# Kernel tuning notes

Hardware: AMD Instinct MI355X
Metric: run time of the kernel (lower is better)

The kernel has to match this reference:

```python
import jax, jax.numpy as jnp
import numpy as np

CUBE_SIZE = 24
N_NEURONS = CUBE_SIZE ** 3  # 13824
INPUT_DIM = 512
OUTPUT_DIM = 1000
MAX_STEPS = 30
BATCH = 256


def _build_neighbor_indices(size: int) -> np.ndarray:
    """[N, 27] int32; invalid (out-of-cube) neighbors map to pad slot N."""
    n = size ** 3
    c = np.arange(size)
    z, y, x = np.meshgrid(c, c, c, indexing='ij')  # each [size,size,size]
    cols = []
    for dz in (-1, 0, 1):
        for dy in (-1, 0, 1):
            for dx in (-1, 0, 1):
                nz, ny, nx = z + dz, y + dy, x + dx
                valid = ((nz >= 0) & (nz < size) & (ny >= 0) & (ny < size)
                         & (nx >= 0) & (nx < size))
                idx = nz * size * size + ny * size + nx
                cols.append(np.where(valid, idx, n))
    return np.stack(cols, axis=-1).reshape(n, 27).astype(np.int32)


def setup_inputs() -> dict:
    key = jax.random.key(0)
    ks = jax.random.split(key, 4)
    # xavier-ish small init scales (gain 0.5 style)
    w_in = jax.random.normal(ks[0], (N_NEURONS, INPUT_DIM), jnp.float32) * 0.01
    w_local = jax.random.normal(ks[1], (N_NEURONS, 27), jnp.float32) * 0.1
    w_out = jax.random.normal(ks[2], (OUTPUT_DIM, N_NEURONS), jnp.float32) * 0.01
    x = jax.random.normal(ks[3], (BATCH, INPUT_DIM), jnp.float32)
    return {
        'x': x,
        'W_in_w': w_in,
        'W_in_b': jnp.zeros((N_NEURONS,), jnp.float32),
        'W_local': w_local,
        'W_out_w': w_out,
        'W_out_b': jnp.zeros((OUTPUT_DIM,), jnp.float32),
        'neighbor_indices': jnp.asarray(_build_neighbor_indices(CUBE_SIZE)),
    }


def reference(x, W_in_w, W_in_b, W_local, W_out_w, W_out_b, neighbor_indices):
    batch = x.shape[0]
    x_proj = x @ W_in_w.T + W_in_b  # [B, N]
    h0 = jnp.zeros((batch, N_NEURONS), x.dtype)
    pad = jnp.zeros((batch, 1), x.dtype)

    def step(h, _):
        h_padded = jnp.concatenate([h, pad], axis=1)        # [B, N+1]
        nbr = h_padded[:, neighbor_indices]                  # [B, N, 27]
        weighted = jnp.einsum('bnk,nk->bn', nbr, W_local)    # [B, N]
        return jnp.tanh(x_proj + weighted), None

    h, _ = jax.lax.scan(step, h0, None, length=MAX_STEPS)
    return h @ W_out_w.T + W_out_b  # [B, output_dim]
```

## Files before the change

kernel.cpp:

```cpp
#include <hip/hip_runtime.h>
#include <hip/hip_bf16.h>

#define NN   13824
#define BB   256
#define KDIM 512
#define ODIM 1000
#define CUBE 24
#define KS   16

typedef short bf8 __attribute__((ext_vector_type(8)));
typedef float f32x4 __attribute__((ext_vector_type(4)));

__device__ __forceinline__ float fast_tanh(float a) {
    float e = __expf(2.0f * a);
    return 1.0f - 2.0f / (e + 1.0f);
}
__device__ __forceinline__ float bf_lo(unsigned u) { return __uint_as_float(u << 16); }
__device__ __forceinline__ float bf_hi(unsigned u) { return __uint_as_float(u & 0xffff0000u); }
__device__ __forceinline__ unsigned short bf_rne(float f) {
    unsigned u = __float_as_uint(f);
    u += 0x7fffu + ((u >> 16) & 1u);
    return (unsigned short)(u >> 16);
}
__device__ __forceinline__ unsigned pk_bf16(float lo, float hi) {
    union { __hip_bfloat162 h; unsigned u; } cv;
    cv.h = __float22bfloat162_rn(make_float2(lo, hi));
    return cv.u;
}
__device__ __forceinline__ bf8 cvt8(float4 a, float4 b) {
    union { bf8 v; unsigned u[4]; } r;
    r.u[0] = pk_bf16(a.x, a.y);
    r.u[1] = pk_bf16(a.z, a.w);
    r.u[2] = pk_bf16(b.x, b.y);
    r.u[3] = pk_bf16(b.z, b.w);
    return r.v;
}

__global__ __launch_bounds__(256) void xbf_kernel(
    const float* __restrict__ x, unsigned* __restrict__ xb)
{
    int i = blockIdx.x * 256 + threadIdx.x;
    float2 v = *(const float2*)&x[(size_t)i * 2];
    xb[i] = pk_bf16(v.x, v.y);
}

__global__ __launch_bounds__(256) void xproj_mfma(
    const float* __restrict__ w_in, const float* __restrict__ bias,
    const short* __restrict__ xbf, unsigned short* __restrict__ xp,
    unsigned short* __restrict__ h1)
{
    const int tid = threadIdx.x, w = tid >> 6, lane = tid & 63;
    const int quad = lane >> 4, l16 = lane & 15;
    const int n0 = blockIdx.x * 16;
    const float* __restrict__ arow = &w_in[(size_t)(n0 + l16) * KDIM];

    f32x4 acc[4] = {};

    int ka = quad * 8;
    float4 a0 = *(const float4*)&arow[ka];
    float4 a1 = *(const float4*)&arow[ka + 4];
    bf8 bb[4];
#pragma unroll
    for (int j = 0; j < 4; ++j)
        bb[j] = *(const bf8*)&xbf[(size_t)(w * 64 + j * 16 + l16) * KDIM + ka];

    for (int it = 0; it < 16; ++it) {
        float4 na0{}, na1{}; bf8 nb[4] = {};
        if (it < 15) {
            const int nka = ka + 32;
            na0 = *(const float4*)&arow[nka];
            na1 = *(const float4*)&arow[nka + 4];
#pragma unroll
            for (int j = 0; j < 4; ++j)
                nb[j] = *(const bf8*)&xbf[(size_t)(w * 64 + j * 16 + l16) * KDIM + nka];
        }
        bf8 af = cvt8(a0, a1);
#pragma unroll
        for (int j = 0; j < 4; ++j)
            acc[j] = __builtin_amdgcn_mfma_f32_16x16x32_bf16(af, bb[j], acc[j], 0, 0, 0);
        a0 = na0; a1 = na1;
#pragma unroll
        for (int j = 0; j < 4; ++j) bb[j] = nb[j];
        ka += 32;
    }

#pragma unroll
    for (int j = 0; j < 4; ++j) {
        const int b = w * 64 + j * 16 + l16;
#pragma unroll
        for (int r = 0; r < 4; ++r) {
            const int n = n0 + quad * 4 + r;
            const float v = acc[j][r] + bias[n];
            xp[(size_t)n * BB + b] = bf_rne(v);
            h1[(size_t)n * BB + b] = bf_rne(fast_tanh(v));
        }
    }
}

__device__ __forceinline__ void load_plane_f2(
    const unsigned* __restrict__ h32, int z, int y, int xx, int dof, float2* w9)
{
#pragma unroll
    for (int j = 0; j < 9; ++j) {
        const int dz = j / 3 - 1, dy = j % 3 - 1;
        const int zz = z + dz, yy = y + dy;
        const bool valid = (xx >= 0) & (xx < CUBE) & (zz >= 0) & (zz < CUBE) &
                           (yy >= 0) & (yy < CUBE);
        unsigned v = 0u;
        if (valid) v = h32[(size_t)((zz * 24 + yy) * 24 + xx) * 128 + dof];
        w9[j] = make_float2(bf_lo(v), bf_hi(v));
    }
}

__global__ __launch_bounds__(128) void step_kernel(
    const unsigned* __restrict__ hprev, const unsigned* __restrict__ xp,
    const float* __restrict__ wl, unsigned* __restrict__ hnext)
{
    const int tid  = threadIdx.x;
    const int wv   = __builtin_amdgcn_readfirstlane(tid >> 6);
    const int lane = tid & 63;

    const int bid   = blockIdx.x;
    const int zhi   = bid & 7;
    const int inner = bid >> 3;
    const int y     = inner % 24;
    const int r     = inner / 24;
    const int xc    = r & 3;
    const int zlo   = r >> 2;
    const int z     = zhi * 3 + zlo;

    const int x0   = xc * 6;
    const int dof  = wv * 64 + lane;

    float2 win[5][9];
    load_plane_f2(hprev, z, y, x0 - 1, dof, win[0]);
    load_plane_f2(hprev, z, y, x0,     dof, win[1]);
    load_plane_f2(hprev, z, y, x0 + 1, dof, win[2]);
    load_plane_f2(hprev, z, y, x0 + 2, dof, win[3]);

#pragma unroll
    for (int xi = 0; xi < 6; ++xi) {
        const int x = x0 + xi;
        if (xi <= 3)
            load_plane_f2(hprev, z, y, x + 3, dof, win[(xi + 4) % 5]);

        const int n = (z * 24 + y) * 24 + x;
        const float* __restrict__ wn = &wl[(size_t)n * 27];
        const unsigned xpv = xp[(size_t)n * 128 + dof];
        float2 acc = make_float2(bf_lo(xpv), bf_hi(xpv));

        const float2* pm = win[xi % 5];
        const float2* pc = win[(xi + 1) % 5];
        const float2* pp = win[(xi + 2) % 5];
#pragma unroll
        for (int j = 0; j < 9; ++j) {
            const float w0 = wn[3 * j + 0];
            const float w1 = wn[3 * j + 1];
            const float w2 = wn[3 * j + 2];
            acc.x += w0 * pm[j].x + w1 * pc[j].x + w2 * pp[j].x;
            acc.y += w0 * pm[j].y + w1 * pc[j].y + w2 * pp[j].y;
        }
        hnext[(size_t)n * 128 + dof] = pk_bf16(fast_tanh(acc.x), fast_tanh(acc.y));
    }
}

__global__ __launch_bounds__(256) void transpose_kernel(
    const unsigned* __restrict__ h32, unsigned* __restrict__ hT32)
{
    __shared__ unsigned short T[64][66];
    const int tid = threadIdx.x;
    const int rr = tid >> 2, g = tid & 3;
    const int k0 = blockIdx.x * 64, b0 = blockIdx.y * 64;
#pragma unroll
    for (int i = 0; i < 8; ++i) {
        unsigned d = h32[(size_t)(k0 + rr) * 128 + b0 / 2 + g * 8 + i];
        const int bl = (g * 8 + i) * 2;
        T[bl][rr]     = (unsigned short)(d & 0xffffu);
        T[bl + 1][rr] = (unsigned short)(d >> 16);
    }
    __syncthreads();
#pragma unroll
    for (int i = 0; i < 8; ++i) {
        const int kl = (g * 8 + i) * 2;
        unsigned d = (unsigned)T[rr][kl] | ((unsigned)T[rr][kl + 1] << 16);
        hT32[(size_t)(b0 + rr) * (NN / 2) + k0 / 2 + g * 8 + i] = d;
    }
}

__global__ __launch_bounds__(256) void outgemm_mfma(
    const float* __restrict__ wout, const short* __restrict__ hT,
    float* __restrict__ part)
{
    const int tid = threadIdx.x, w = tid >> 6, lane = tid & 63;
    const int quad = lane >> 4, l16 = lane & 15;
    const int o0 = blockIdx.x * 32;
    const int kb = blockIdx.y * (NN / KS);
    const int b0 = w * 64;

    const int oa = o0 + l16, ob = o0 + 16 + l16;
    const bool av0 = oa < ODIM, av1 = ob < ODIM;
    const float* __restrict__ ar0 = &wout[(size_t)oa * NN];
    const float* __restrict__ ar1 = &wout[(size_t)ob * NN];
    const float4 z4 = {0.f, 0.f, 0.f, 0.f};

    f32x4 acc[2][4] = {};

    int ka = kb + quad * 8;
    float4 a00 = av0 ? *(const float4*)&ar0[ka]     : z4;
    float4 a01 = av0 ? *(const float4*)&ar0[ka + 4] : z4;
    float4 a10 = av1 ? *(const float4*)&ar1[ka]     : z4;
    float4 a11 = av1 ? *(const float4*)&ar1[ka + 4] : z4;
    bf8 bb[4];
#pragma unroll
    for (int j = 0; j < 4; ++j)
        bb[j] = *(const bf8*)&hT[(size_t)(b0 + j * 16 + l16) * NN + ka];

    for (int it = 0; it < 27; ++it) {
        float4 na00{}, na01{}, na10{}, na11{}; bf8 nb[4] = {};
        if (it < 26) {
            const int nka = ka + 32;
            na00 = av0 ? *(const float4*)&ar0[nka]     : z4;
            na01 = av0 ? *(const float4*)&ar0[nka + 4] : z4;
            na10 = av1 ? *(const float4*)&ar1[nka]     : z4;
            na11 = av1 ? *(const float4*)&ar1[nka + 4] : z4;
#pragma unroll
            for (int j = 0; j < 4; ++j)
                nb[j] = *(const bf8*)&hT[(size_t)(b0 + j * 16 + l16) * NN + nka];
        }
        bf8 af0 = cvt8(a00, a01);
        bf8 af1 = cvt8(a10, a11);
#pragma unroll
        for (int j = 0; j < 4; ++j) {
            acc[0][j] = __builtin_amdgcn_mfma_f32_16x16x32_bf16(af0, bb[j], acc[0][j], 0, 0, 0);
            acc[1][j] = __builtin_amdgcn_mfma_f32_16x16x32_bf16(af1, bb[j], acc[1][j], 0, 0, 0);
        }
        a00 = na00; a01 = na01; a10 = na10; a11 = na11;
#pragma unroll
        for (int j = 0; j < 4; ++j) bb[j] = nb[j];
        ka += 32;
    }

#pragma unroll
    for (int i = 0; i < 2; ++i)
#pragma unroll
        for (int j = 0; j < 4; ++j) {
            const int b = b0 + j * 16 + l16;
#pragma unroll
            for (int r = 0; r < 4; ++r) {
                const int o = o0 + i * 16 + quad * 4 + r;
                part[((size_t)blockIdx.y * 1024 + o) * BB + b] = acc[i][j][r];
            }
        }
}

__global__ __launch_bounds__(256) void reduce_kernel(
    const float* __restrict__ part, const float* __restrict__ bias,
    float* __restrict__ out)
{
    const int o = blockIdx.x, b = threadIdx.x;
    float s = bias[o];
#pragma unroll
    for (int kc = 0; kc < KS; ++kc)
        s += part[((size_t)kc * 1024 + o) * BB + b];
    out[(size_t)b * ODIM + o] = s;
}

extern "C" void kernel_launch(void* const* d_in, const int* in_sizes, int n_in,
                              void* d_out, int out_size, void* d_ws, size_t ws_size,
                              hipStream_t stream)
{
    const float* x       = (const float*)d_in[0];
    const float* w_in    = (const float*)d_in[1];
    const float* b_in    = (const float*)d_in[2];
    const float* w_local = (const float*)d_in[3];
    const float* w_out   = (const float*)d_in[4];
    const float* b_out   = (const float*)d_in[5];
    float* out = (float*)d_out;

    char* p = (char*)d_ws;
    unsigned short* xp_bf = (unsigned short*)p;          p += (size_t)NN * BB * 2;
    unsigned short* hA    = (unsigned short*)p;          p += (size_t)NN * BB * 2;
    unsigned short* hB    = (unsigned short*)p;          p += (size_t)NN * BB * 2;
    unsigned short* hT    = (unsigned short*)p;          p += (size_t)NN * BB * 2;
    unsigned short* x_bf  = (unsigned short*)p;          p += (size_t)BB * KDIM * 2;
    float*          part  = (float*)p;

    xbf_kernel<<<256, 256, 0, stream>>>(x, (unsigned*)x_bf);
    xproj_mfma<<<864, 256, 0, stream>>>(w_in, b_in, (const short*)x_bf, xp_bf, hA);

    const unsigned* hp = (const unsigned*)hA;
    unsigned* hn = (unsigned*)hB;
    for (int s = 0; s < 29; ++s) {
        step_kernel<<<2304, 128, 0, stream>>>(hp, (const unsigned*)xp_bf, w_local, hn);
        unsigned* t = (unsigned*)hp; hp = hn; hn = t;
    }

    transpose_kernel<<<dim3(216, 4), 256, 0, stream>>>(hp, (unsigned*)hT);
    outgemm_mfma<<<dim3(32, KS), 256, 0, stream>>>(w_out, (const short*)hT, part);
    reduce_kernel<<<ODIM, 256, 0, stream>>>(part, b_out, out);
}
```

Baseline: 573.5 us.

## Widen step-kernel x strip, keep planes packed, and retile output GEMM

The stencil step kernel now gives each block 8 x-positions instead of 6, so there are 1728 blocks. Neighbour planes stay as packed bf16 words and are unpacked only when used, and all xp values are prefetched up front. The inner sum is split into three independent accumulators, and a launch-bounds occupancy hint is added. The output GEMM is retiled to 16 output rows per block with a two-stage register prefetch and a fully unrolled K loop, doubling the grid. Together these aim to cut halo reloads and register pressure, raise occupancy and improve memory-latency hiding, at the risk of a different tail balance and occupancy.

```diff
diff --git a/kernel.cpp b/kernel.cpp
--- a/kernel.cpp
+++ b/kernel.cpp
@@ -97,8 +97,9 @@
     }
 }
 
-__device__ __forceinline__ void load_plane_f2(
-    const unsigned* __restrict__ h32, int z, int y, int xx, int dof, float2* w9)
+__device__ __forceinline__ void load_plane_pk(
+    const unsigned* __restrict__ h32, int z, int y, int xx, int dof,
+    unsigned* pk)
 {
 #pragma unroll
     for (int j = 0; j < 9; ++j) {
@@ -108,11 +109,16 @@
                            (yy >= 0) & (yy < CUBE);
         unsigned v = 0u;
         if (valid) v = h32[(size_t)((zz * 24 + yy) * 24 + xx) * 128 + dof];
-        w9[j] = make_float2(bf_lo(v), bf_hi(v));
-    }
-}
-
-__global__ __launch_bounds__(128) void step_kernel(
+        pk[j] = v;
+    }
+}
+__device__ __forceinline__ void unpack9(const unsigned* pk, float2* u) {
+#pragma unroll
+    for (int j = 0; j < 9; ++j)
+        u[j] = make_float2(bf_lo(pk[j]), bf_hi(pk[j]));
+}
+
+__global__ __launch_bounds__(128, 4) void step_kernel(
     const unsigned* __restrict__ hprev, const unsigned* __restrict__ xp,
     const float* __restrict__ wl, unsigned* __restrict__ hnext)
 {
@@ -125,42 +131,58 @@
     const int inner = bid >> 3;
     const int y     = inner % 24;
     const int r     = inner / 24;
-    const int xc    = r & 3;
-    const int zlo   = r >> 2;
+    const int xc    = r % 3;
+    const int zlo   = r / 3;
     const int z     = zhi * 3 + zlo;
 
-    const int x0   = xc * 6;
-    const int dof  = wv * 64 + lane;
-
-    float2 win[5][9];
-    load_plane_f2(hprev, z, y, x0 - 1, dof, win[0]);
-    load_plane_f2(hprev, z, y, x0,     dof, win[1]);
-    load_plane_f2(hprev, z, y, x0 + 1, dof, win[2]);
-    load_plane_f2(hprev, z, y, x0 + 2, dof, win[3]);
-
-#pragma unroll
-    for (int xi = 0; xi < 6; ++xi) {
-        const int x = x0 + xi;
-        if (xi <= 3)
-            load_plane_f2(hprev, z, y, x + 3, dof, win[(xi + 4) % 5]);
-
-        const int n = (z * 24 + y) * 24 + x;
+    const int x0  = xc * 8;
+    const int dof = wv * 64 + lane;
+    const int n0  = (z * 24 + y) * 24 + x0;
+
+    unsigned pk[2][9];
+    unsigned tm[9], tc[9];
+    float2   u[3][9];
+
+    load_plane_pk(hprev, z, y, x0 - 1, dof, tm);
+    load_plane_pk(hprev, z, y, x0,     dof, tc);
+    load_plane_pk(hprev, z, y, x0 + 1, dof, pk[0]);
+    load_plane_pk(hprev, z, y, x0 + 2, dof, pk[1]);
+
+    unsigned xpv[8];
+#pragma unroll
+    for (int xi = 0; xi < 8; ++xi)
+        xpv[xi] = xp[(size_t)(n0 + xi) * 128 + dof];
+
+    unpack9(tm, u[0]);
+    unpack9(tc, u[1]);
+
+#pragma unroll
+    for (int xi = 0; xi < 8; ++xi) {
+        unpack9(pk[xi & 1], u[(xi + 2) % 3]);
+        if (xi <= 5)
+            load_plane_pk(hprev, z, y, x0 + xi + 3, dof, pk[xi & 1]);
+
+        const int n = n0 + xi;
         const float* __restrict__ wn = &wl[(size_t)n * 27];
-        const unsigned xpv = xp[(size_t)n * 128 + dof];
-        float2 acc = make_float2(bf_lo(xpv), bf_hi(xpv));
-
-        const float2* pm = win[xi % 5];
-        const float2* pc = win[(xi + 1) % 5];
-        const float2* pp = win[(xi + 2) % 5];
+        const float2* pm = u[xi % 3];
+        const float2* pc = u[(xi + 1) % 3];
+        const float2* pp = u[(xi + 2) % 3];
+
+        float2 a0 = make_float2(bf_lo(xpv[xi]), bf_hi(xpv[xi]));
+        float2 a1 = make_float2(0.f, 0.f);
+        float2 a2 = make_float2(0.f, 0.f);
 #pragma unroll
         for (int j = 0; j < 9; ++j) {
             const float w0 = wn[3 * j + 0];
             const float w1 = wn[3 * j + 1];
             const float w2 = wn[3 * j + 2];
-            acc.x += w0 * pm[j].x + w1 * pc[j].x + w2 * pp[j].x;
-            acc.y += w0 * pm[j].y + w1 * pc[j].y + w2 * pp[j].y;
-        }
-        hnext[(size_t)n * 128 + dof] = pk_bf16(fast_tanh(acc.x), fast_tanh(acc.y));
+            a0.x += w0 * pm[j].x; a0.y += w0 * pm[j].y;
+            a1.x += w1 * pc[j].x; a1.y += w1 * pc[j].y;
+            a2.x += w2 * pp[j].x; a2.y += w2 * pp[j].y;
+        }
+        const float sx = a0.x + a1.x + a2.x;
+        const float sy = a0.y + a1.y + a2.y;
+        hnext[(size_t)n * 128 + dof] = pk_bf16(fast_tanh(sx), fast_tanh(sy));
     }
 }
 
@@ -193,64 +215,56 @@
 {
     const int tid = threadIdx.x, w = tid >> 6, lane = tid & 63;
     const int quad = lane >> 4, l16 = lane & 15;
-    const int o0 = blockIdx.x * 32;
+    const int o0 = blockIdx.x * 16;
     const int kb = blockIdx.y * (NN / KS);
     const int b0 = w * 64;
 
-    const int oa = o0 + l16, ob = o0 + 16 + l16;
-    const bool av0 = oa < ODIM, av1 = ob < ODIM;
-    const float* __restrict__ ar0 = &wout[(size_t)oa * NN];
-    const float* __restrict__ ar1 = &wout[(size_t)ob * NN];
+    const int oa = o0 + l16;
+    const bool av = oa < ODIM;
+    const float* __restrict__ ar = &wout[(size_t)oa * NN];
     const float4 z4 = {0.f, 0.f, 0.f, 0.f};
 
-    f32x4 acc[2][4] = {};
-
-    int ka = kb + quad * 8;
-    float4 a00 = av0 ? *(const float4*)&ar0[ka]     : z4;
-    float4 a01 = av0 ? *(const float4*)&ar0[ka + 4] : z4;
-    float4 a10 = av1 ? *(const float4*)&ar1[ka]     : z4;
-    float4 a11 = av1 ? *(const float4*)&ar1[ka + 4] : z4;
-    bf8 bb[4];
-#pragma unroll
-    for (int j = 0; j < 4; ++j)
-        bb[j] = *(const bf8*)&hT[(size_t)(b0 + j * 16 + l16) * NN + ka];
-
+    f32x4 acc[4] = {};
+
+    float4 A0[2], A1[2];
+    bf8    Bv[2][4];
+
+#pragma unroll
+    for (int s = 0; s < 2; ++s) {
+        const int ka = kb + s * 32 + quad * 8;
+        A0[s] = av ? *(const float4*)&ar[ka]     : z4;
+        A1[s] = av ? *(const float4*)&ar[ka + 4] : z4;
+#pragma unroll
+        for (int j = 0; j < 4; ++j)
+            Bv[s][j] = *(const bf8*)&hT[(size_t)(b0 + j * 16 + l16) * NN + ka];
+    }
+
+#pragma unroll
     for (int it = 0; it < 27; ++it) {
-        float4 na00{}, na01{}, na10{}, na11{}; bf8 nb[4] = {};
-        if (it < 26) {
-            const int nka = ka + 32;
-            na00 = av0 ? *(const float4*)&ar0[nka]     : z4;
-            na01 = av0 ? *(const float4*)&ar0[nka + 4] : z4;
-            na10 = av1 ? *(const float4*)&ar1[nka]     : z4;
-            na11 = av1 ? *(const float4*)&ar1[nka + 4] : z4;
+        const int s = it & 1;
+        bf8 af = cvt8(A0[s], A1[s]);
+#pragma unroll
+        for (int j = 0; j < 4; ++j)
+            acc[j] = __builtin_amdgcn_mfma_f32_16x16x32_bf16(af, Bv[s][j], acc[j], 0, 0, 0);
+        if (it + 2 < 27) {
+            const int ka = kb + (it + 2) * 32 + quad * 8;
+            A0[s] = av ? *(const float4*)&ar[ka]     : z4;
+            A1[s] = av ? *(const float4*)&ar[ka + 4] : z4;
 #pragma unroll
             for (int j = 0; j < 4; ++j)
-                nb[j] = *(const bf8*)&hT[(size_t)(b0 + j * 16 + l16) * NN + nka];
-        }
-        bf8 af0 = cvt8(a00, a01);
-        bf8 af1 = cvt8(a10, a11);
-#pragma unroll
-        for (int j = 0; j < 4; ++j) {
-            acc[0][j] = __builtin_amdgcn_mfma_f32_16x16x32_bf16(af0, bb[j], acc[0][j], 0, 0, 0);
-            acc[1][j] = __builtin_amdgcn_mfma_f32_16x16x32_bf16(af1, bb[j], acc[1][j], 0, 0, 0);
-        }
-        a00 = na00; a01 = na01; a10 = na10; a11 = na11;
-#pragma unroll
-        for (int j = 0; j < 4; ++j) bb[j] = nb[j];
-        ka += 32;
-    }
-
-#pragma unroll
-    for (int i = 0; i < 2; ++i)
-#pragma unroll
-        for (int j = 0; j < 4; ++j) {
-            const int b = b0 + j * 16 + l16;
-#pragma unroll
-            for (int r = 0; r < 4; ++r) {
-                const int o = o0 + i * 16 + quad * 4 + r;
-                part[((size_t)blockIdx.y * 1024 + o) * BB + b] = acc[i][j][r];
-            }
-        }
+                Bv[s][j] = *(const bf8*)&hT[(size_t)(b0 + j * 16 + l16) * NN + ka];
+        }
+    }
+
+#pragma unroll
+    for (int j = 0; j < 4; ++j) {
+        const int b = b0 + j * 16 + l16;
+#pragma unroll
+        for (int r = 0; r < 4; ++r) {
+            const int o = o0 + quad * 4 + r;
+            part[((size_t)blockIdx.y * 1024 + o) * BB + b] = acc[j][r];
+        }
+    }
 }
 
 __global__ __launch_bounds__(256) void reduce_kernel(
@@ -291,11 +305,11 @@
     const unsigned* hp = (const unsigned*)hA;
     unsigned* hn = (unsigned*)hB;
     for (int s = 0; s < 29; ++s) {
-        step_kernel<<<2304, 128, 0, stream>>>(hp, (const unsigned*)xp_bf, w_local, hn);
+        step_kernel<<<1728, 128, 0, stream>>>(hp, (const unsigned*)xp_bf, w_local, hn);
         unsigned* t = (unsigned*)hp; hp = hn; hn = t;
     }
 
     transpose_kernel<<<dim3(216, 4), 256, 0, stream>>>(hp, (unsigned*)hT);
-    outgemm_mfma<<<dim3(32, KS), 256, 0, stream>>>(w_out, (const short*)hT, part);
+    outgemm_mfma<<<dim3(63, KS), 256, 0, stream>>>(w_out, (const short*)hT, part);
     reduce_kernel<<<ODIM, 256, 0, stream>>>(part, b_out, out);
 }
```

Measured after the change: 685.0 us. +19.4%, slower.
